# Optimization experiments

Hardware: AMD Instinct MI355X
Metric: run time of the kernel (lower is better)

The kernel has to match this reference:

```python
import jax, jax.numpy as jnp
import numpy as np

T, HID = 2048, 1536
H, DK, DV = 12, 128, 128
KEY_DIM, VAL_DIM = H * DK, H * DV
CONV_K, GEN_RED = 4, 8
EPS = 1e-5


def setup_inputs() -> dict:
    key = jax.random.key(0)
    ks = jax.random.split(key, 12)
    def rn(k, sh, scale):
        return jax.random.normal(k, sh, dtype=jnp.float32) * scale
    inv = HID ** -0.5
    return {
        "hidden_states": rn(ks[0], (T, HID), 1.0),
        "Wq": rn(ks[1], (HID, KEY_DIM), inv),
        "Wk": rn(ks[2], (HID, KEY_DIM), inv),
        "Wv": rn(ks[3], (HID, VAL_DIM), inv),
        "Wb": rn(ks[4], (HID, H), inv),
        "Wa": rn(ks[5], (HID, H), inv),
        "A_log": jnp.log(jax.random.uniform(ks[6], (H,), minval=1e-3, maxval=16.0)),
        "dt_bias": jnp.ones((H,), jnp.float32),
        "Wg1": rn(ks[7], (HID, HID // GEN_RED), inv),
        "Wg2": rn(ks[8], (HID // GEN_RED, VAL_DIM * CONV_K), (HID // GEN_RED) ** -0.5),
        "Wgate": rn(ks[9], (HID, VAL_DIM), inv),
        "norm_weight": jnp.ones((DV,), jnp.float32),
        "Wo": rn(ks[10], (VAL_DIM, HID), VAL_DIM ** -0.5),
    }


def _dynamic_conv(v, hs, Wg1, Wg2):
    # per-token per-channel causal depthwise conv; kernels generated from hidden_states
    w = jax.nn.silu(hs @ Wg1) @ Wg2                    # (T, VAL_DIM*K)
    w = w.reshape(T, VAL_DIM, CONV_K)                  # (T, D, K)
    vpad = jnp.pad(v, ((CONV_K - 1, 0), (0, 0)))       # causal left pad
    windows = jnp.stack([vpad[i:i + T] for i in range(CONV_K)], axis=1)  # (T, K, D)
    return jax.nn.silu(jnp.einsum('tkd,tdk->td', windows, w))


def _gated_delta_rule(q, k, v, g, beta):
    # q,k: (T,H,DK); v: (T,H,DV); g,beta: (T,H)
    scale = DK ** -0.5
    def step(S, inp):
        q_t, k_t, v_t, g_t, b_t = inp
        S = S * jnp.exp(g_t)[:, None, None]            # decay state
        kv = jnp.einsum('hk,hkv->hv', k_t, S)          # k^T S
        S = S + jnp.einsum('hk,hv->hkv', k_t, (v_t - kv) * b_t[:, None])
        o_t = jnp.einsum('hk,hkv->hv', q_t, S) * scale
        return S, o_t
    S0 = jnp.zeros((H, DK, DV), jnp.float32)
    _, o = jax.lax.scan(step, S0, (q, k, v, g, beta))
    return o                                           # (T, H, DV)


def reference(hidden_states, Wq, Wk, Wv, Wb, Wa, A_log, dt_bias,
              Wg1, Wg2, Wgate, norm_weight, Wo):
    hs = hidden_states
    q = jax.nn.silu(hs @ Wq).reshape(T, H, DK)
    k = jax.nn.silu(hs @ Wk).reshape(T, H, DK)
    v = _dynamic_conv(hs @ Wv, hs, Wg1, Wg2).reshape(T, H, DV)
    beta = jax.nn.sigmoid(hs @ Wb)                           # (T, H)
    g = -jnp.exp(A_log) * jax.nn.softplus(hs @ Wa + dt_bias)  # (T, H) log-decay
    o = _gated_delta_rule(q, k, v, g, beta)                  # (T, H, DV)
    # gated RMSNorm over head_v_dim
    gate = (hs @ Wgate).reshape(T, H, DV)
    o = o * jax.lax.rsqrt(jnp.mean(o * o, axis=-1, keepdims=True) + EPS)
    o = o * norm_weight * (gate * jax.nn.sigmoid(gate))
    return o.reshape(T, VAL_DIM) @ Wo
```

## Files before the change

kernel.cpp:

```cpp
#include <hip/hip_runtime.h>
#include <hip/hip_bf16.h>
#include <math.h>

#define T     2048
#define HID   1536
#define NH    12
#define DK    128
#define DV    128
#define CONVK 4
#define CH    64
#define NC    32

typedef __attribute__((ext_vector_type(8))) short bf16x8;
typedef __attribute__((ext_vector_type(8))) _Float16 fp16x8;
typedef __attribute__((ext_vector_type(4))) float floatx4;

__device__ __forceinline__ float siluf(float x) {
    return x / (1.0f + __expf(-x));
}
__device__ __forceinline__ unsigned short f2bf(float f) {
    union { __hip_bfloat16 b; unsigned short u; } cv;
    cv.b = __float2bfloat16(f);
    return cv.u;
}
__device__ __forceinline__ float bf2f(unsigned short u) {
    union { unsigned int u; float f; } cv;
    cv.u = ((unsigned int)u) << 16;
    return cv.f;
}
__device__ __forceinline__ unsigned short f2h(float f) {
    union { _Float16 h; unsigned short u; } cv;
    cv.h = (_Float16)f;
    return cv.u;
}
__device__ __forceinline__ void gl_lds16(const void* g, void* l) {
    __builtin_amdgcn_global_load_lds(
        (const __attribute__((address_space(1))) void*)g,
        (__attribute__((address_space(3))) void*)l, 16, 0, 0);
}
__device__ __forceinline__ void split8_store(const float* xv,
                                             unsigned short* dh, unsigned short* dl) {
    ushort4 h0, h1, l0, l1;
    h0.x = f2bf(xv[0]); l0.x = f2bf(xv[0] - bf2f(h0.x));
    h0.y = f2bf(xv[1]); l0.y = f2bf(xv[1] - bf2f(h0.y));
    h0.z = f2bf(xv[2]); l0.z = f2bf(xv[2] - bf2f(h0.z));
    h0.w = f2bf(xv[3]); l0.w = f2bf(xv[3] - bf2f(h0.w));
    h1.x = f2bf(xv[4]); l1.x = f2bf(xv[4] - bf2f(h1.x));
    h1.y = f2bf(xv[5]); l1.y = f2bf(xv[5] - bf2f(h1.y));
    h1.z = f2bf(xv[6]); l1.z = f2bf(xv[6] - bf2f(h1.z));
    h1.w = f2bf(xv[7]); l1.w = f2bf(xv[7] - bf2f(h1.w));
    *(ushort4*)dh = h0; *(ushort4*)(dh + 4) = h1;
    *(ushort4*)dl = l0; *(ushort4*)(dl + 4) = l1;
}

__global__ __launch_bounds__(256) void splitcast3_kernel(const float* __restrict__ s,
                                                         unsigned short* __restrict__ hi,
                                                         unsigned short* __restrict__ lo,
                                                         unsigned short* __restrict__ h16,
                                                         int n4) {
    int i = blockIdx.x * 256 + threadIdx.x;
    if (i >= n4) return;
    float4 x = ((const float4*)s)[i];
    ushort4 h, l, f;
    h.x = f2bf(x.x); l.x = f2bf(x.x - bf2f(h.x)); f.x = f2h(x.x);
    h.y = f2bf(x.y); l.y = f2bf(x.y - bf2f(h.y)); f.y = f2h(x.y);
    h.z = f2bf(x.z); l.z = f2bf(x.z - bf2f(h.z)); f.z = f2h(x.z);
    h.w = f2bf(x.w); l.w = f2bf(x.w - bf2f(h.w)); f.w = f2h(x.w);
    ((ushort4*)hi)[i] = h;
    ((ushort4*)lo)[i] = l;
    ((ushort4*)h16)[i] = f;
}

__global__ __launch_bounds__(256) void transsplit_kernel(const float* __restrict__ src,
                                                         unsigned short* __restrict__ hi,
                                                         unsigned short* __restrict__ lo,
                                                         int K, int N) {
    __shared__ float tile[32][33];
    const int k0 = blockIdx.y * 32, n0 = blockIdx.x * 32;
    const int tx = threadIdx.x, ty = threadIdx.y;
#pragma unroll
    for (int r = 0; r < 4; ++r) {
        int kk = k0 + ty + 8 * r, nn = n0 + tx;
        tile[ty + 8 * r][tx] = (nn < N) ? src[(size_t)kk * N + nn] : 0.0f;
    }
    __syncthreads();
#pragma unroll
    for (int r = 0; r < 4; ++r) {
        int nn = n0 + ty + 8 * r, kk = k0 + tx;
        if (nn < N) {
            float x = tile[tx][ty + 8 * r];
            unsigned short h = f2bf(x);
            hi[(size_t)nn * K + kk] = h;
            lo[(size_t)nn * K + kk] = f2bf(x - bf2f(h));
        }
    }
}

__global__ __launch_bounds__(256) void transcasth_kernel(const float* __restrict__ src,
                                                         unsigned short* __restrict__ dst,
                                                         int K, int N) {
    __shared__ float tile[32][33];
    const int k0 = blockIdx.y * 32, n0 = blockIdx.x * 32;
    const int tx = threadIdx.x, ty = threadIdx.y;
#pragma unroll
    for (int r = 0; r < 4; ++r) {
        int kk = k0 + ty + 8 * r, nn = n0 + tx;
        tile[ty + 8 * r][tx] = (nn < N) ? src[(size_t)kk * N + nn] : 0.0f;
    }
    __syncthreads();
#pragma unroll
    for (int r = 0; r < 4; ++r) {
        int nn = n0 + ty + 8 * r, kk = k0 + tx;
        if (nn < N) dst[(size_t)nn * K + kk] = f2h(tile[tx][ty + 8 * r]);
    }
}

template<int EPI, int MODE>
__global__ __launch_bounds__(256)
void mgemm(const unsigned short* __restrict__ Ah, const unsigned short* __restrict__ Al,
           const unsigned short* __restrict__ Bh, const unsigned short* __restrict__ Bl,
           int K, int N, float* __restrict__ C, unsigned short* __restrict__ Cb)
{
    constexpr int BN   = MODE ? 64 : 128;
    constexpr int BCH  = BN / 16;
    constexpr int NFR  = MODE ? 2 : 4;
    __shared__ unsigned short AsH[2][4096];
    __shared__ unsigned short BsH[2][BCH * 512];
    __shared__ unsigned short AsL[MODE ? 2 : 1][MODE ? 4096 : 4];
    __shared__ unsigned short BsL[MODE ? 2 : 1][MODE ? BCH * 512 : 4];
    const int tid = threadIdx.x;
    const int wave = tid >> 6, lane = tid & 63;
    const int wr = wave >> 1, wc = wave & 1;
    const int lm = lane & 15, lq = lane >> 4;
    const int rowBase = blockIdx.y * 128, colBase = blockIdx.x * BN;

    floatx4 acc[4][NFR];
#pragma unroll
    for (int i = 0; i < 4; ++i)
#pragma unroll
        for (int j = 0; j < NFR; ++j) acc[i][j] = (floatx4){0.f, 0.f, 0.f, 0.f};

    const int mt0 = wave * 2, mt1 = wave * 2 + 1;
    const size_t aOff0 = (size_t)(rowBase + mt0 * 16 + lm) * K + lq * 8;
    const size_t aOff1 = (size_t)(rowBase + mt1 * 16 + lm) * K + lq * 8;
    const size_t bOff0 = (size_t)(colBase + mt0 * 16 + lm) * K + lq * 8;
    const size_t bOff1 = (size_t)(colBase + mt1 * 16 + lm) * K + lq * 8;
    const size_t bOffW = (size_t)(colBase + wave * 16 + lm) * K + lq * 8;

    auto STAGE = [&](int buf, int k0) {
        gl_lds16(Ah + aOff0 + k0, &AsH[buf][mt0 * 512]);
        gl_lds16(Ah + aOff1 + k0, &AsH[buf][mt1 * 512]);
        if (MODE) {
            gl_lds16(Al + aOff0 + k0, &AsL[buf][mt0 * 512]);
            gl_lds16(Al + aOff1 + k0, &AsL[buf][mt1 * 512]);
            gl_lds16(Bh + bOffW + k0, &BsH[buf][wave * 512]);
            gl_lds16(Bl + bOffW + k0, &BsL[buf][wave * 512]);
        } else {
            gl_lds16(Bh + bOff0 + k0, &BsH[buf][mt0 * 512]);
            gl_lds16(Bh + bOff1 + k0, &BsH[buf][mt1 * 512]);
        }
    };

    const int nIter = K >> 5;
    STAGE(0, 0);
    __syncthreads();
    int cur = 0;
    for (int it = 0; it < nIter; ++it) {
        if (it + 1 < nIter) STAGE(cur ^ 1, (it + 1) << 5);
        if (MODE == 0) {
            fp16x8 a[4], b[4];
#pragma unroll
            for (int i = 0; i < 4; ++i) {
                a[i] = *(const fp16x8*)&AsH[cur][(wr * 4 + i) * 512 + lane * 8];
                b[i] = *(const fp16x8*)&BsH[cur][(wc * 4 + i) * 512 + lane * 8];
            }
#pragma unroll
            for (int mi = 0; mi < 4; ++mi)
#pragma unroll
                for (int ni = 0; ni < 4; ++ni)
                    acc[mi][ni] = __builtin_amdgcn_mfma_f32_16x16x32_f16(
                        a[mi], b[ni], acc[mi][ni], 0, 0, 0);
        } else {
            bf16x8 ah[4], al[4], bh[2], bl[2];
#pragma unroll
            for (int i = 0; i < 4; ++i) {
                ah[i] = *(const bf16x8*)&AsH[cur][(wr * 4 + i) * 512 + lane * 8];
                al[i] = *(const bf16x8*)&AsL[cur][(wr * 4 + i) * 512 + lane * 8];
            }
#pragma unroll
            for (int j = 0; j < 2; ++j) {
                bh[j] = *(const bf16x8*)&BsH[cur][(wc * 2 + j) * 512 + lane * 8];
                bl[j] = *(const bf16x8*)&BsL[cur][(wc * 2 + j) * 512 + lane * 8];
            }
#pragma unroll
            for (int mi = 0; mi < 4; ++mi)
#pragma unroll
                for (int ni = 0; ni < 2; ++ni) {
                    acc[mi][ni] = __builtin_amdgcn_mfma_f32_16x16x32_bf16(
                        ah[mi], bh[ni], acc[mi][ni], 0, 0, 0);
                    acc[mi][ni] = __builtin_amdgcn_mfma_f32_16x16x32_bf16(
                        al[mi], bh[ni], acc[mi][ni], 0, 0, 0);
                    acc[mi][ni] = __builtin_amdgcn_mfma_f32_16x16x32_bf16(
                        ah[mi], bl[ni], acc[mi][ni], 0, 0, 0);
                }
        }
        __syncthreads();
        cur ^= 1;
    }

#pragma unroll
    for (int mi = 0; mi < 4; ++mi)
#pragma unroll
        for (int ni = 0; ni < NFR; ++ni) {
            const int col = colBase + wc * (NFR * 16) + ni * 16 + lm;
#pragma unroll
            for (int r = 0; r < 4; ++r) {
                const int row = rowBase + wr * 64 + mi * 16 + lq * 4 + r;
                const float x = acc[mi][ni][r];
                if (EPI == 0) C[(size_t)row * N + col] = x;
                else          Cb[(size_t)row * N + col] = f2bf(x);
            }
        }
}

__global__ __launch_bounds__(256)
void mgemm_ab(const unsigned short* __restrict__ Ah0, const unsigned short* __restrict__ Bh0,
              const unsigned short* __restrict__ Ah1, const unsigned short* __restrict__ Al1,
              const unsigned short* __restrict__ Bh1, const unsigned short* __restrict__ Bl1,
              float* __restrict__ qf, float* __restrict__ vf,
              unsigned short* __restrict__ gsilb, unsigned short* __restrict__ w1h16,
              float* __restrict__ kf,
              const float* __restrict__ A_log, const float* __restrict__ dt_bias,
              float* __restrict__ beta, float* __restrict__ g)
{
    __shared__ unsigned short smem[24576];
    const int tid = threadIdx.x;
    const int wave = tid >> 6, lane = tid & 63;
    const int wr = wave >> 1, wc = wave & 1;
    const int lm = lane & 15, lq = lane >> 4;
    const int K = 1536;
    const int bx = blockIdx.x;

    bool roleA; int aidx = 0, bidx = 0;
    if (bx < 832) { roleA = ((bx & 1) == 0); aidx = bx >> 1; bidx = bx >> 1; }
    else          { roleA = true;            aidx = 416 + (bx - 832); }

    const int mt0 = wave * 2, mt1 = wave * 2 + 1;

    if (roleA) {
        const int rowBase = (aidx / 38) * 128, colBase = (aidx % 38) * 128;
        unsigned short* AsH = smem;
        unsigned short* BsH = smem + 8192;
        floatx4 acc[4][4];
#pragma unroll
        for (int i = 0; i < 4; ++i)
#pragma unroll
            for (int j = 0; j < 4; ++j) acc[i][j] = (floatx4){0.f, 0.f, 0.f, 0.f};

        const size_t aOff0 = (size_t)(rowBase + mt0 * 16 + lm) * K + lq * 8;
        const size_t aOff1 = (size_t)(rowBase + mt1 * 16 + lm) * K + lq * 8;
        const size_t bOff0 = (size_t)(colBase + mt0 * 16 + lm) * K + lq * 8;
        const size_t bOff1 = (size_t)(colBase + mt1 * 16 + lm) * K + lq * 8;

        auto STAGE = [&](int buf, int k0) {
            gl_lds16(Ah0 + aOff0 + k0, &AsH[buf * 4096 + mt0 * 512]);
            gl_lds16(Ah0 + aOff1 + k0, &AsH[buf * 4096 + mt1 * 512]);
            gl_lds16(Bh0 + bOff0 + k0, &BsH[buf * 4096 + mt0 * 512]);
// ... 222 lines not shown
    const int wave = tid >> 6, lane = tid & 63;
    const int lm = lane & 15, lq = lane >> 4;
    const int li = tid >> 2, lq4 = tid & 3;
    const size_t rowbase = (size_t)(c * CH) * HID + h * DK;

    {
        const float* ksrc = k + rowbase + (size_t)li * HID + lq4 * 32;
        const float* qsrc = q + rowbase + (size_t)li * HID + lq4 * 32;
        const float* vsrc = v + (size_t)(c * CH + li) * HID + h * DV + lq4 * 32;
#pragma unroll
        for (int f = 0; f < 8; ++f) {
            float4 kx = *(const float4*)(ksrc + f * 4);
            float4 qx = *(const float4*)(qsrc + f * 4);
            float4 vx = *(const float4*)(vsrc + f * 4);
            const int d0 = lq4 * 32 + f * 4;
            {
                ushort4 hh, ll;
                hh.x = f2bf(kx.x); ll.x = f2bf(kx.x - bf2f(hh.x));
                hh.y = f2bf(kx.y); ll.y = f2bf(kx.y - bf2f(hh.y));
                hh.z = f2bf(kx.z); ll.z = f2bf(kx.z - bf2f(hh.z));
                hh.w = f2bf(kx.w); ll.w = f2bf(kx.w - bf2f(hh.w));
                *(ushort4*)&KhS[li * 136 + d0] = hh;
                *(ushort4*)&KlS[li * 136 + d0] = ll;
            }
            {
                ushort4 hh, ll;
                hh.x = f2bf(qx.x); ll.x = f2bf(qx.x - bf2f(hh.x));
                hh.y = f2bf(qx.y); ll.y = f2bf(qx.y - bf2f(hh.y));
                hh.z = f2bf(qx.z); ll.z = f2bf(qx.z - bf2f(hh.z));
                hh.w = f2bf(qx.w); ll.w = f2bf(qx.w - bf2f(hh.w));
                *(ushort4*)&QhS[li * 136 + d0] = hh;
                *(ushort4*)&QlS[li * 136 + d0] = ll;
            }
            KT[(d0 + 0) * 68 + li] = kx.x;
            KT[(d0 + 1) * 68 + li] = kx.y;
            KT[(d0 + 2) * 68 + li] = kx.z;
            KT[(d0 + 3) * 68 + li] = kx.w;
            *(float4*)&Vs[li * 132 + d0] = vx;
        }
    }
    if (tid < 64) {
        float gv = g[(c * CH + tid) * NH + h];
        float bv = beta[(c * CH + tid) * NH + h];
        float csv = gv;
#pragma unroll
        for (int off = 1; off < 64; off <<= 1) {
            float n = __shfl_up(csv, off);
            if (tid >= off) csv += n;
        }
        cs[tid] = csv; sb[tid] = bv; sbb[tid] = bv * __expf(csv);
    }
    __syncthreads();

    {
        const int ti = wave;
#pragma unroll
        for (int tj = 0; tj < 4; ++tj) {
            floatx4 acc = (floatx4){0.f, 0.f, 0.f, 0.f};
#pragma unroll
            for (int ks = 0; ks < 4; ++ks) {
                bf16x8 a_h = *(const bf16x8*)&KhS[(ti * 16 + lm) * 136 + ks * 32 + lq * 8];
                bf16x8 a_l = *(const bf16x8*)&KlS[(ti * 16 + lm) * 136 + ks * 32 + lq * 8];
                bf16x8 b_h = *(const bf16x8*)&KhS[(tj * 16 + lm) * 136 + ks * 32 + lq * 8];
                bf16x8 b_l = *(const bf16x8*)&KlS[(tj * 16 + lm) * 136 + ks * 32 + lq * 8];
                acc = __builtin_amdgcn_mfma_f32_16x16x32_bf16(a_h, b_h, acc, 0, 0, 0);
                acc = __builtin_amdgcn_mfma_f32_16x16x32_bf16(a_h, b_l, acc, 0, 0, 0);
                acc = __builtin_amdgcn_mfma_f32_16x16x32_bf16(a_l, b_h, acc, 0, 0, 0);
            }
#pragma unroll
            for (int r = 0; r < 4; ++r) {
                const int i = ti * 16 + lq * 4 + r, j = tj * 16 + lm;
                As[i * 68 + j] = (j < i) ? sb[i] * __expf(cs[i] - cs[j]) * acc[r] : 0.0f;
            }
        }
        const size_t mbase = (size_t)(h * NC + c) * CH * CH;
#pragma unroll
        for (int tj = 0; tj < 4; ++tj) {
            floatx4 acc = (floatx4){0.f, 0.f, 0.f, 0.f};
#pragma unroll
            for (int ks = 0; ks < 4; ++ks) {
                bf16x8 a_h = *(const bf16x8*)&QhS[(ti * 16 + lm) * 136 + ks * 32 + lq * 8];
                bf16x8 a_l = *(const bf16x8*)&QlS[(ti * 16 + lm) * 136 + ks * 32 + lq * 8];
                bf16x8 b_h = *(const bf16x8*)&KhS[(tj * 16 + lm) * 136 + ks * 32 + lq * 8];
                bf16x8 b_l = *(const bf16x8*)&KlS[(tj * 16 + lm) * 136 + ks * 32 + lq * 8];
                acc = __builtin_amdgcn_mfma_f32_16x16x32_bf16(a_h, b_h, acc, 0, 0, 0);
                acc = __builtin_amdgcn_mfma_f32_16x16x32_bf16(a_h, b_l, acc, 0, 0, 0);
                acc = __builtin_amdgcn_mfma_f32_16x16x32_bf16(a_l, b_h, acc, 0, 0, 0);
            }
#pragma unroll
            for (int r = 0; r < 4; ++r) {
                const int i = ti * 16 + lq * 4 + r, j = tj * 16 + lm;
                Mg[mbase + (size_t)i * 64 + j] =
                    (j <= i) ? __expf(cs[i] - cs[j]) * acc[r] : 0.0f;
            }
        }
    }

    float xc[64];
    const int col = tid;
    if (col < 128) {
#pragma unroll
        for (int i = 0; i < 64; ++i) xc[i] = sb[i] * Vs[i * 132 + col];
    } else {
        const int dcol = col - 128;
#pragma unroll
        for (int i4 = 0; i4 < 16; ++i4) {
            float4 kq = *(const float4*)&KT[dcol * 68 + i4 * 4];
            xc[i4 * 4 + 0] = sbb[i4 * 4 + 0] * kq.x;
            xc[i4 * 4 + 1] = sbb[i4 * 4 + 1] * kq.y;
            xc[i4 * 4 + 2] = sbb[i4 * 4 + 2] * kq.z;
            xc[i4 * 4 + 3] = sbb[i4 * 4 + 3] * kq.w;
        }
    }
    __syncthreads();

#pragma unroll
    for (int i = 1; i < 64; ++i) {
        float a = xc[i];
#pragma unroll
        for (int j4 = 0; j4 < (i + 3) / 4; ++j4) {
            float4 a4 = *(const float4*)&As[i * 68 + j4 * 4];
            a -= a4.x * xc[j4 * 4 + 0] + a4.y * xc[j4 * 4 + 1]
               + a4.z * xc[j4 * 4 + 2] + a4.w * xc[j4 * 4 + 3];
        }
        xc[i] = a;
    }

    {
        const size_t xbase = (size_t)(h * NC + c) * CH * 128;
        if (col < 128) {
            for (int i = 0; i < 64; ++i) X1g[xbase + (size_t)i * 128 + col] = xc[i];
        } else {
            for (int i = 0; i < 64; ++i) Vs[i * 132 + (col - 128)] = xc[i];
        }
    }
    if (tid < 64) csg[(size_t)(h * NC + c) * CH + tid] = cs[tid];
    __syncthreads();

    const size_t tb = (size_t)(h * NC + c) * 8192;

    {
#pragma unroll
        for (int e = 0; e < 4; ++e) {
            int u = e * 256 + tid;
            int ch = u >> 6, l = u & 63;
            int i = (ch >> 2) * 16 + (l & 15);
            int dbase = (ch & 3) * 32 + (l >> 4) * 8;
            float4 a = *(const float4*)&Vs[i * 132 + dbase];
            float4 b = *(const float4*)&Vs[i * 132 + dbase + 4];
            float xv[8] = {-a.x, -a.y, -a.z, -a.w, -b.x, -b.y, -b.z, -b.w};
            split8_store(xv, &X2th[tb + ch * 512 + l * 8], &X2tl[tb + ch * 512 + l * 8]);
        }
    }

    {
#pragma unroll
        for (int e = 0; e < 4; ++e) {
            int u = e * 256 + tid;
            int ch = u >> 6, l = u & 63;
            int i = (ch >> 2) * 16 + (l & 15);
            int dbase = (ch & 3) * 32 + (l >> 4) * 8;
            *(bf16x8*)&Qth[tb + ch * 512 + l * 8] = *(const bf16x8*)&QhS[i * 136 + dbase];
            *(bf16x8*)&Qtl[tb + ch * 512 + l * 8] = *(const bf16x8*)&QlS[i * 136 + dbase];
        }
    }

    {
#pragma unroll
        for (int e = 0; e < 4; ++e) {
            int u = e * 256 + tid;
            int ch = u >> 6, l = u & 63;
            int dk = (ch >> 1) * 16 + (l & 15);
            int ibase = (ch & 1) * 32 + (l >> 4) * 8;
            float4 a = *(const float4*)&KT[dk * 68 + ibase];
            float4 b = *(const float4*)&KT[dk * 68 + ibase + 4];
            float xv[8] = {a.x, a.y, a.z, a.w, b.x, b.y, b.z, b.w};
            split8_store(xv, &Kth[tb + ch * 512 + l * 8], &Ktl[tb + ch * 512 + l * 8]);
        }
    }
}

struct StFrags {
    bf16x8 xh[4], xl[4], qh[4], ql[4], kh[4], kl[4];
    float x1r[4], csr[4], cs63;
};

__device__ __forceinline__ void st_load(
    StFrags& f,
    const unsigned short* __restrict__ Qth, const unsigned short* __restrict__ Qtl,
    const unsigned short* __restrict__ Kth, const unsigned short* __restrict__ Ktl,
    const unsigned short* __restrict__ X2th, const unsigned short* __restrict__ X2tl,
    const float* __restrict__ X1g, const float* __restrict__ csg,
    int h, int c, int db, int mw, int lane, int lq, int lm)
{
    const size_t hc = (size_t)(h * NC + c);
    const size_t xb = hc * CH * 128;
    const size_t tb = hc * 8192 + (size_t)lane * 8;
#pragma unroll
    for (int ks = 0; ks < 4; ++ks) {
        const size_t off = tb + (size_t)(mw * 4 + ks) * 512;
        f.xh[ks] = *(const bf16x8*)(X2th + off);
        f.xl[ks] = *(const bf16x8*)(X2tl + off);
        f.qh[ks] = *(const bf16x8*)(Qth + off);
        f.ql[ks] = *(const bf16x8*)(Qtl + off);
        f.kh[ks] = *(const bf16x8*)(Kth + off);
        f.kl[ks] = *(const bf16x8*)(Ktl + off);
    }
#pragma unroll
    for (int r = 0; r < 4; ++r) {
        const int row = mw * 16 + lq * 4 + r;
        f.x1r[r] = X1g[xb + (size_t)row * 128 + db * 16 + lm];
        f.csr[r] = csg[hc * CH + row];
    }
    f.cs63 = csg[hc * CH + 63];
}

__device__ __forceinline__ void st_compute(
    const StFrags& f, floatx4& st0, floatx4& st1,
    unsigned short* SBh, unsigned short* SBl,
    unsigned short* UBh, unsigned short* UBl,
    float* __restrict__ X1g, float* __restrict__ o,
    int h, int c, int db, int mw, int lane, int lq, int lm)
{
    const size_t hc = (size_t)(h * NC + c);
    const size_t xb = hc * CH * 128;

    {
        floatx4 aU0 = (floatx4){0.f, 0.f, 0.f, 0.f};
        floatx4 aU1 = (floatx4){0.f, 0.f, 0.f, 0.f};
        floatx4 aO0 = (floatx4){0.f, 0.f, 0.f, 0.f};
        floatx4 aO1 = (floatx4){0.f, 0.f, 0.f, 0.f};
#pragma unroll
        for (int ks = 0; ks < 4; ++ks) {
            bf16x8 sh = *(const bf16x8*)&SBh[lm * 136 + ks * 32 + lq * 8];
            bf16x8 sl = *(const bf16x8*)&SBl[lm * 136 + ks * 32 + lq * 8];
            if (ks & 1) {
                aU1 = __builtin_amdgcn_mfma_f32_16x16x32_bf16(f.xh[ks], sh, aU1, 0, 0, 0);
                aU1 = __builtin_amdgcn_mfma_f32_16x16x32_bf16(f.xh[ks], sl, aU1, 0, 0, 0);
                aU1 = __builtin_amdgcn_mfma_f32_16x16x32_bf16(f.xl[ks], sh, aU1, 0, 0, 0);
                aO1 = __builtin_amdgcn_mfma_f32_16x16x32_bf16(f.qh[ks], sh, aO1, 0, 0, 0);
                aO1 = __builtin_amdgcn_mfma_f32_16x16x32_bf16(f.qh[ks], sl, aO1, 0, 0, 0);
                aO1 = __builtin_amdgcn_mfma_f32_16x16x32_bf16(f.ql[ks], sh, aO1, 0, 0, 0);
            } else {
                aU0 = __builtin_amdgcn_mfma_f32_16x16x32_bf16(f.xh[ks], sh, aU0, 0, 0, 0);
                aU0 = __builtin_amdgcn_mfma_f32_16x16x32_bf16(f.xh[ks], sl, aU0, 0, 0, 0);
                aU0 = __builtin_amdgcn_mfma_f32_16x16x32_bf16(f.xl[ks], sh, aU0, 0, 0, 0);
                aO0 = __builtin_amdgcn_mfma_f32_16x16x32_bf16(f.qh[ks], sh, aO0, 0, 0, 0);
                aO0 = __builtin_amdgcn_mfma_f32_16x16x32_bf16(f.qh[ks], sl, aO0, 0, 0, 0);
                aO0 = __builtin_amdgcn_mfma_f32_16x16x32_bf16(f.ql[ks], sh, aO0, 0, 0, 0);
            }
        }
#pragma unroll
        for (int r = 0; r < 4; ++r) {
            const int row = mw * 16 + lq * 4 + r;
            const float u = aU0[r] + aU1[r] + f.x1r[r];
            X1g[xb + (size_t)row * 128 + db * 16 + lm] = u;
            const float up = u * __expf(f.cs63 - f.csr[r]);
            unsigned short uh = f2bf(up);
            UBh[lm * 72 + row] = uh;
            UBl[lm * 72 + row] = f2bf(up - bf2f(uh));
            o[(size_t)(c * CH + row) * HID + h * DV + db * 16 + lm] =
                __expf(f.csr[r]) * (aO0[r] + aO1[r]);
        }
    }
    __syncthreads();

    {
        const float bC = __expf(f.cs63);
#pragma unroll
        for (int mt2 = 0; mt2 < 2; ++mt2) {
            const int mt = mw * 2 + mt2;
            floatx4 acc;
            floatx4 stc = mt2 ? st1 : st0;
#pragma unroll
            for (int r = 0; r < 4; ++r) acc[r] = bC * stc[r];
#pragma unroll
            for (int ks = 0; ks < 2; ++ks) {
                bf16x8 ah = f.kh[mt2 * 2 + ks];
                bf16x8 al = f.kl[mt2 * 2 + ks];
                bf16x8 bh = *(const bf16x8*)&UBh[lm * 72 + ks * 32 + lq * 8];
                bf16x8 bl = *(const bf16x8*)&UBl[lm * 72 + ks * 32 + lq * 8];
                acc = __builtin_amdgcn_mfma_f32_16x16x32_bf16(ah, bh, acc, 0, 0, 0);
                acc = __builtin_amdgcn_mfma_f32_16x16x32_bf16(ah, bl, acc, 0, 0, 0);
                acc = __builtin_amdgcn_mfma_f32_16x16x32_bf16(al, bh, acc, 0, 0, 0);
            }
            if (mt2) st1 = acc; else st0 = acc;
            ushort4 shv, slv;
#pragma unroll
            for (int r = 0; r < 4; ++r) {
                const float sv = acc[r];
                unsigned short sh = f2bf(sv);
                ((unsigned short*)&shv)[r] = sh;
                ((unsigned short*)&slv)[r] = f2bf(sv - bf2f(sh));
            }
            const int dkb = mt * 16 + lq * 4;
            *(ushort4*)&SBh[lm * 136 + dkb] = shv;
            *(ushort4*)&SBl[lm * 136 + dkb] = slv;
        }
    }
    __syncthreads();
}

__global__ __launch_bounds__(256, 1) void state_kernel(
    const unsigned short* __restrict__ Qth, const unsigned short* __restrict__ Qtl,
    const unsigned short* __restrict__ Kth, const unsigned short* __restrict__ Ktl,
    const unsigned short* __restrict__ X2th, const unsigned short* __restrict__ X2tl,
    float* __restrict__ X1g ,
    const float* __restrict__ csg, float* __restrict__ o)
{
    __shared__ unsigned short SBh[16 * 136], SBl[16 * 136];
    __shared__ unsigned short UBh[16 * 72],  UBl[16 * 72];

    const int h = blockIdx.x, db = blockIdx.y;
    const int tid = threadIdx.x;
    const int mw = tid >> 6, lane = tid & 63;
    const int lm = lane & 15, lq = lane >> 4;

    for (int idx = tid; idx < 16 * 136; idx += 256) { SBh[idx] = 0; SBl[idx] = 0; }
    floatx4 st0 = (floatx4){0.f, 0.f, 0.f, 0.f};
    floatx4 st1 = (floatx4){0.f, 0.f, 0.f, 0.f};
    __syncthreads();

    StFrags fA, fB;
    st_load(fA, Qth, Qtl, Kth, Ktl, X2th, X2tl, X1g, csg, h, 0, db, mw, lane, lq, lm);
    for (int c = 0; c < NC; c += 2) {
        st_load(fB, Qth, Qtl, Kth, Ktl, X2th, X2tl, X1g, csg, h, c + 1, db, mw, lane, lq, lm);
        __builtin_amdgcn_sched_barrier(0);
        st_compute(fA, st0, st1, SBh, SBl, UBh, UBl, X1g, o, h, c, db, mw, lane, lq, lm);
        if (c + 2 < NC)
            st_load(fA, Qth, Qtl, Kth, Ktl, X2th, X2tl, X1g, csg, h, c + 2, db, mw, lane, lq, lm);
        __builtin_amdgcn_sched_barrier(0);
        st_compute(fB, st0, st1, SBh, SBl, UBh, UBl, X1g, o, h, c + 1, db, mw, lane, lq, lm);
    }
}

__global__ __launch_bounds__(256) void outk_kernel(
    const float* __restrict__ Ug, const float* __restrict__ Mg,
    float* __restrict__ o)
{
    __shared__ float Msh[64 * 68];
    __shared__ float Ush[64 * 68];

    const int c = blockIdx.x, h = blockIdx.y;
    const int dvb = blockIdx.z * 64;
    const int tid = threadIdx.x;
    const size_t hc = (size_t)(h * NC + c);

    for (int e = 0; e < 16; ++e) {
        int idx = e * 256 + tid;
        Msh[(idx >> 6) * 68 + (idx & 63)] = Mg[hc * CH * CH + idx];
    }
    for (int e = 0; e < 16; ++e) {
        int idx = e * 256 + tid;
        int j = idx >> 6, cc = idx & 63;
        Ush[j * 68 + cc] = Ug[hc * CH * 128 + (size_t)j * 128 + dvb + cc];
    }
    __syncthreads();

    const int tx = tid & 15, ty = tid >> 4;
    const int c0 = tx * 4, i0 = ty * 4;
    float acc[4][4] = {{0}};
    for (int j4 = 0; j4 < 16; ++j4) {
        float uv[4][4];
#pragma unroll
        for (int s = 0; s < 4; ++s) {
            float4 u4 = *(const float4*)&Ush[(j4 * 4 + s) * 68 + c0];
            uv[s][0] = u4.x; uv[s][1] = u4.y; uv[s][2] = u4.z; uv[s][3] = u4.w;
        }
#pragma unroll
        for (int r = 0; r < 4; ++r) {
            float4 m4 = *(const float4*)&Msh[(i0 + r) * 68 + j4 * 4];
            const float mv[4] = {m4.x, m4.y, m4.z, m4.w};
#pragma unroll
            for (int s = 0; s < 4; ++s)
#pragma unroll
                for (int e = 0; e < 4; ++e) acc[r][e] += mv[s] * uv[s][e];
        }
    }
    const float scale = 0.08838834764831845f;
#pragma unroll
    for (int r = 0; r < 4; ++r) {
        float* op = &o[(size_t)(c * CH + i0 + r) * HID + h * DV + dvb + c0];
        float4 prev = *(const float4*)op;
        float4 ov = make_float4(scale * (prev.x + acc[r][0]),
                                scale * (prev.y + acc[r][1]),
                                scale * (prev.z + acc[r][2]),
                                scale * (prev.w + acc[r][3]));
        *(float4*)op = ov;
    }
}

__global__ __launch_bounds__(256) void normgate_kernel(const float* __restrict__ o,
                                                       const unsigned short* __restrict__ gsil,
                                                       const float* __restrict__ nw,
                                                       unsigned short* __restrict__ out_hi,
                                                       unsigned short* __restrict__ out_lo) {
    const int gw = (blockIdx.x * 256 + threadIdx.x) >> 6;
    const int lane = threadIdx.x & 63;
    if (gw >= T * NH) return;
    const int t = gw / NH, h = gw % NH;
    const size_t base = (size_t)t * HID + h * DV;
    const float a = o[base + lane];
    const float b = o[base + lane + 64];
    float ss = a * a + b * b;
    ss += __shfl_xor(ss, 1);  ss += __shfl_xor(ss, 2);  ss += __shfl_xor(ss, 4);
    ss += __shfl_xor(ss, 8);  ss += __shfl_xor(ss, 16); ss += __shfl_xor(ss, 32);
    const float r = rsqrtf(ss * (1.0f / 128.0f) + 1e-5f);
    float va = a * r * nw[lane]      * bf2f(gsil[base + lane]);
    float vb = b * r * nw[lane + 64] * bf2f(gsil[base + lane + 64]);
    unsigned short ha = f2bf(va), hb = f2bf(vb);
    out_hi[base + lane]      = ha;  out_lo[base + lane]      = f2bf(va - bf2f(ha));
    out_hi[base + lane + 64] = hb;  out_lo[base + lane + 64] = f2bf(vb - bf2f(hb));
}

extern "C" void kernel_launch(void* const* d_in, const int* in_sizes, int n_in,
                              void* d_out, int out_size, void* d_ws, size_t ws_size,
                              hipStream_t stream) {
    const float* hs      = (const float*)d_in[0];
    const float* Wq      = (const float*)d_in[1];
    const float* Wk      = (const float*)d_in[2];
    const float* Wv      = (const float*)d_in[3];
    const float* Wb      = (const float*)d_in[4];
    const float* Wa      = (const float*)d_in[5];
    const float* A_log   = (const float*)d_in[6];
    const float* dt_bias = (const float*)d_in[7];
    const float* Wg1     = (const float*)d_in[8];
    const float* Wg2     = (const float*)d_in[9];
    const float* Wgate   = (const float*)d_in[10];
    const float* norm_w  = (const float*)d_in[11];
    const float* Wo      = (const float*)d_in[12];

    float* ws = (float*)d_ws;
    float* q    = ws;
    float* kbuf = ws + 3145728;
    float* vpre = ws + 6291456;
    float* vbuf = ws + 9437184;
    unsigned short* gsil = (unsigned short*)(ws + 12582912);
    float* X1g  = ws + 14155776;
    unsigned short* X2th = (unsigned short*)(ws + 17301504);
    unsigned short* X2tl = (unsigned short*)(ws + 18874368);
    float* Mg   = ws + 20447232;
    unsigned short* WTAfh = (unsigned short*)(ws + 14155776);
    unsigned short* WTBh  = (unsigned short*)(ws + 17891328);
    unsigned short* WTBl  = (unsigned short*)(ws + 19169280);
    unsigned short* WG2h  = (unsigned short*)(ws + 22044672);
    unsigned short* hsh   = (unsigned short*)(ws + 22634496);
    unsigned short* w1h16 = (unsigned short*)(ws + 24207360);
    unsigned short* Kth = (unsigned short*)(ws + 22044672);
    unsigned short* Ktl = (unsigned short*)(ws + 23617536);
    float* beta  = ws + 25190400;
    float* g     = ws + 25214976;
    float* csg   = ws + 25239552;
    unsigned short* hsbh = (unsigned short*)(ws + 9437184);
    unsigned short* hsbl = (unsigned short*)(ws + 11010048);
    unsigned short* Qth  = (unsigned short*)(ws + 6291456);
    unsigned short* Qtl  = (unsigned short*)(ws + 7864320);
    unsigned short* WoTh = (unsigned short*)(ws);
    unsigned short* WoTl = (unsigned short*)(ws + 1179648);
    unsigned short* onh  = (unsigned short*)(ws + 6291456);
    unsigned short* onl  = (unsigned short*)(ws + 7864320);

    const dim3 blk(256);
    const dim3 blkT(32, 8);

    splitcast3_kernel<<<3072, blk, 0, stream>>>(hs, hsbh, hsbl, hsh, (T * HID) / 4);
    transcasth_kernel<<<dim3(48, 48), blkT, 0, stream>>>(Wq,    WTAfh,               1536, 1536);
    transcasth_kernel<<<dim3(48, 48), blkT, 0, stream>>>(Wv,    WTAfh + 1536 * 1536, 1536, 1536);
    transcasth_kernel<<<dim3(48, 48), blkT, 0, stream>>>(Wgate, WTAfh + 3072 * 1536, 1536, 1536);
    transcasth_kernel<<<dim3(6, 48),  blkT, 0, stream>>>(Wg1,   WTAfh + 4608 * 1536, 1536, 192);
    transsplit_kernel<<<dim3(48, 48), blkT, 0, stream>>>(Wk, WTBh,               WTBl,               1536, 1536);
    transsplit_kernel<<<dim3(1, 48),  blkT, 0, stream>>>(Wb, WTBh + 1536 * 1536, WTBl + 1536 * 1536, 1536, 12);
    transsplit_kernel<<<dim3(1, 48),  blkT, 0, stream>>>(Wa, WTBh + 1548 * 1536, WTBl + 1548 * 1536, 1536, 12);
    transcasth_kernel<<<dim3(192, 6), blkT, 0, stream>>>(Wg2, WG2h, 192, 6144);

    mgemm_ab<<<1024, blk, 0, stream>>>(hsh, WTAfh, hsbh, hsbl, WTBh, WTBl,
                                       q, vpre, gsil, w1h16, kbuf,
                                       A_log, dt_bias, beta, g);

    convgemm<<<dim3(48, 16), blk, 0, stream>>>(w1h16, WG2h, vpre, vbuf);

    chunkloc_kernel<<<dim3(NC, NH), blk, 0, stream>>>(q, kbuf, vbuf, g, beta,
                                                      X1g, X2th, X2tl, Mg, csg,
                                                      Qth, Qtl, Kth, Ktl);
    state_kernel<<<dim3(NH, 8), blk, 0, stream>>>(Qth, Qtl, Kth, Ktl, X2th, X2tl,
                                                  X1g, csg, vbuf);
    transsplit_kernel<<<dim3(48, 48), blkT, 0, stream>>>(Wo, WoTh, WoTl, 1536, 1536);
    outk_kernel<<<dim3(NC, NH, 2), blk, 0, stream>>>(X1g, Mg, vbuf);

    normgate_kernel<<<6144, blk, 0, stream>>>(vbuf, gsil, norm_w, onh, onl);
    mgemm<0, 1><<<dim3(24, 16), blk, 0, stream>>>(onh, onl, WoTh, WoTl, 1536, 1536,
        (float*)d_out, nullptr);
}
```

Before: 551.6 us.

## Merge weight-prep launches into one kernel and fuse output correction with gated RMSNorm

The nine separate cast/transpose launches for hidden states and weights are folded into a single prep_all kernel that dispatches on block index ranges. The intra-chunk output correction kernel now covers the full 128-wide value dimension per block, so it can compute the RMS norm and gate in shared memory. That removes the separate normgate kernel and its round trip through global memory. In exchange, the output kernel launches half as many blocks, each using more registers and shared memory, which lowers parallelism.

Result: faster. 532.4 us (-3.5%).

```diff
diff --git a/kernel.cpp b/kernel.cpp
--- a/kernel.cpp
+++ b/kernel.cpp
@@ -53,66 +53,109 @@
     *(ushort4*)dl = l0; *(ushort4*)(dl + 4) = l1;
 }
 
-__global__ __launch_bounds__(256) void splitcast3_kernel(const float* __restrict__ s,
-                                                         unsigned short* __restrict__ hi,
-                                                         unsigned short* __restrict__ lo,
-                                                         unsigned short* __restrict__ h16,
-                                                         int n4) {
-    int i = blockIdx.x * 256 + threadIdx.x;
-    if (i >= n4) return;
-    float4 x = ((const float4*)s)[i];
-    ushort4 h, l, f;
-    h.x = f2bf(x.x); l.x = f2bf(x.x - bf2f(h.x)); f.x = f2h(x.x);
-    h.y = f2bf(x.y); l.y = f2bf(x.y - bf2f(h.y)); f.y = f2h(x.y);
-    h.z = f2bf(x.z); l.z = f2bf(x.z - bf2f(h.z)); f.z = f2h(x.z);
-    h.w = f2bf(x.w); l.w = f2bf(x.w - bf2f(h.w)); f.w = f2h(x.w);
-    ((ushort4*)hi)[i] = h;
-    ((ushort4*)lo)[i] = l;
-    ((ushort4*)h16)[i] = f;
+__device__ __forceinline__ void tch_body(const float* __restrict__ src,
+                                         unsigned short* __restrict__ dst,
+                                         int K, int N, int gx, int gy, int tid,
+                                         float* tile ) {
+    const int tx = tid & 31, ty = tid >> 5;
+    const int k0 = gy * 32, n0 = gx * 32;
+#pragma unroll
+    for (int r = 0; r < 4; ++r) {
+        int kk = k0 + ty + 8 * r, nn = n0 + tx;
+        tile[(ty + 8 * r) * 33 + tx] = (nn < N) ? src[(size_t)kk * N + nn] : 0.0f;
+    }
+    __syncthreads();
+#pragma unroll
+    for (int r = 0; r < 4; ++r) {
+        int nn = n0 + ty + 8 * r, kk = k0 + tx;
+        if (nn < N) dst[(size_t)nn * K + kk] = f2h(tile[tx * 33 + ty + 8 * r]);
+    }
+}
+__device__ __forceinline__ void tsp_body(const float* __restrict__ src,
+                                         unsigned short* __restrict__ hi,
+                                         unsigned short* __restrict__ lo,
+                                         int K, int N, int gx, int gy, int tid,
+                                         float* tile) {
+    const int tx = tid & 31, ty = tid >> 5;
+    const int k0 = gy * 32, n0 = gx * 32;
+#pragma unroll
+    for (int r = 0; r < 4; ++r) {
+        int kk = k0 + ty + 8 * r, nn = n0 + tx;
+        tile[(ty + 8 * r) * 33 + tx] = (nn < N) ? src[(size_t)kk * N + nn] : 0.0f;
+    }
+    __syncthreads();
+#pragma unroll
+    for (int r = 0; r < 4; ++r) {
+        int nn = n0 + ty + 8 * r, kk = k0 + tx;
+        if (nn < N) {
+            float x = tile[tx * 33 + ty + 8 * r];
+            unsigned short h = f2bf(x);
+            hi[(size_t)nn * K + kk] = h;
+            lo[(size_t)nn * K + kk] = f2bf(x - bf2f(h));
+        }
+    }
+}
+
+__global__ __launch_bounds__(256) void prep_all(
+    const float* __restrict__ hs,
+    unsigned short* __restrict__ hsbh, unsigned short* __restrict__ hsbl,
+    unsigned short* __restrict__ hsh,
+    const float* __restrict__ Wq, const float* __restrict__ Wv,
+    const float* __restrict__ Wgate, const float* __restrict__ Wg1,
+    const float* __restrict__ Wg2,
+    const float* __restrict__ Wk, const float* __restrict__ Wb,
+    const float* __restrict__ Wa,
+    unsigned short* __restrict__ WTAfh, unsigned short* __restrict__ WG2h,
+    unsigned short* __restrict__ WTBh, unsigned short* __restrict__ WTBl)
+{
+    __shared__ float tile[32 * 33];
+    const int bx = blockIdx.x, tid = threadIdx.x;
+
+    if (bx < 3072) {
+        const int i = bx * 256 + tid;
+        float4 x = ((const float4*)hs)[i];
+        ushort4 h, l, f;
+        h.x = f2bf(x.x); l.x = f2bf(x.x - bf2f(h.x)); f.x = f2h(x.x);
+        h.y = f2bf(x.y); l.y = f2bf(x.y - bf2f(h.y)); f.y = f2h(x.y);
+        h.z = f2bf(x.z); l.z = f2bf(x.z - bf2f(h.z)); f.z = f2h(x.z);
+        h.w = f2bf(x.w); l.w = f2bf(x.w - bf2f(h.w)); f.w = f2h(x.w);
+        ((ushort4*)hsbh)[i] = h;
+        ((ushort4*)hsbl)[i] = l;
+        ((ushort4*)hsh)[i]  = f;
+    } else if (bx < 5376) {
+        const int t = bx - 3072;
+        tch_body(Wq, WTAfh, 1536, 1536, t % 48, t / 48, tid, tile);
+    } else if (bx < 7680) {
+        const int t = bx - 5376;
+        tch_body(Wv, WTAfh + 1536 * 1536, 1536, 1536, t % 48, t / 48, tid, tile);
+    } else if (bx < 9984) {
+        const int t = bx - 7680;
+        tch_body(Wgate, WTAfh + 3072 * 1536, 1536, 1536, t % 48, t / 48, tid, tile);
+    } else if (bx < 10272) {
+        const int t = bx - 9984;
+        tch_body(Wg1, WTAfh + 4608 * 1536, 1536, 192, t % 6, t / 6, tid, tile);
+    } else if (bx < 11424) {
+        const int t = bx - 10272;
+        tch_body(Wg2, WG2h, 192, 6144, t % 192, t / 192, tid, tile);
+    } else if (bx < 13728) {
+        const int t = bx - 11424;
+        tsp_body(Wk, WTBh, WTBl, 1536, 1536, t % 48, t / 48, tid, tile);
+    } else if (bx < 13776) {
+        const int t = bx - 13728;
+        tsp_body(Wb, WTBh + 1536 * 1536, WTBl + 1536 * 1536, 1536, 12, 0, t, tid, tile);
+    } else {
+        const int t = bx - 13776;
+        tsp_body(Wa, WTBh + 1548 * 1536, WTBl + 1548 * 1536, 1536, 12, 0, t, tid, tile);
+    }
 }
 
 __global__ __launch_bounds__(256) void transsplit_kernel(const float* __restrict__ src,
                                                          unsigned short* __restrict__ hi,
                                                          unsigned short* __restrict__ lo,
                                                          int K, int N) {
-    __shared__ float tile[32][33];
-    const int k0 = blockIdx.y * 32, n0 = blockIdx.x * 32;
-    const int tx = threadIdx.x, ty = threadIdx.y;
-#pragma unroll
-    for (int r = 0; r < 4; ++r) {
-        int kk = k0 + ty + 8 * r, nn = n0 + tx;
-        tile[ty + 8 * r][tx] = (nn < N) ? src[(size_t)kk * N + nn] : 0.0f;
-    }
-    __syncthreads();
-#pragma unroll
-    for (int r = 0; r < 4; ++r) {
-        int nn = n0 + ty + 8 * r, kk = k0 + tx;
-        if (nn < N) {
-            float x = tile[tx][ty + 8 * r];
-            unsigned short h = f2bf(x);
-            hi[(size_t)nn * K + kk] = h;
-            lo[(size_t)nn * K + kk] = f2bf(x - bf2f(h));
-        }
-    }
-}
-
-__global__ __launch_bounds__(256) void transcasth_kernel(const float* __restrict__ src,
-                                                         unsigned short* __restrict__ dst,
-                                                         int K, int N) {
-    __shared__ float tile[32][33];
-    const int k0 = blockIdx.y * 32, n0 = blockIdx.x * 32;
-    const int tx = threadIdx.x, ty = threadIdx.y;
-#pragma unroll
-    for (int r = 0; r < 4; ++r) {
-        int kk = k0 + ty + 8 * r, nn = n0 + tx;
-        tile[ty + 8 * r][tx] = (nn < N) ? src[(size_t)kk * N + nn] : 0.0f;
-    }
-    __syncthreads();
-#pragma unroll
-    for (int r = 0; r < 4; ++r) {
-        int nn = n0 + ty + 8 * r, kk = k0 + tx;
-        if (nn < N) dst[(size_t)nn * K + kk] = f2h(tile[tx][ty + 8 * r]);
-    }
+    __shared__ float tile[32 * 33];
+    const int tid = (int)(threadIdx.y * blockDim.x + threadIdx.x);
+    tsp_body(src, hi, lo, K, N, blockIdx.x, blockIdx.y, tid, tile);
 }
 
 template<int EPI, int MODE>
@@ -641,7 +684,6 @@
             split8_store(xv, &X2th[tb + ch * 512 + l * 8], &X2tl[tb + ch * 512 + l * 8]);
         }
     }
-
     {
 #pragma unroll
         for (int e = 0; e < 4; ++e) {
@@ -653,7 +695,6 @@
             *(bf16x8*)&Qtl[tb + ch * 512 + l * 8] = *(const bf16x8*)&QlS[i * 136 + dbase];
         }
     }
-
     {
 #pragma unroll
         for (int e = 0; e < 4; ++e) {
@@ -794,8 +835,7 @@
     const unsigned short* __restrict__ Qth, const unsigned short* __restrict__ Qtl,
     const unsigned short* __restrict__ Kth, const unsigned short* __restrict__ Ktl,
     const unsigned short* __restrict__ X2th, const unsigned short* __restrict__ X2tl,
-    float* __restrict__ X1g ,
-    const float* __restrict__ csg, float* __restrict__ o)
+    float* __restrict__ X1g, const float* __restrict__ csg, float* __restrict__ o)
 {
     __shared__ unsigned short SBh[16 * 136], SBl[16 * 136];
     __shared__ unsigned short UBh[16 * 72],  UBl[16 * 72];
@@ -823,15 +863,17 @@
     }
 }
 
-__global__ __launch_bounds__(256) void outk_kernel(
+__global__ __launch_bounds__(256) void outknorm_kernel(
     const float* __restrict__ Ug, const float* __restrict__ Mg,
-    float* __restrict__ o)
+    const float* __restrict__ o ,
+    const unsigned short* __restrict__ gsil, const float* __restrict__ nw,
+    unsigned short* __restrict__ out_hi, unsigned short* __restrict__ out_lo)
 {
     __shared__ float Msh[64 * 68];
-    __shared__ float Ush[64 * 68];
+    __shared__ float Ush[64 * 132];
+    __shared__ float rsq[64];
 
     const int c = blockIdx.x, h = blockIdx.y;
-    const int dvb = blockIdx.z * 64;
     const int tid = threadIdx.x;
     const size_t hc = (size_t)(h * NC + c);
 
@@ -839,22 +881,24 @@
         int idx = e * 256 + tid;
         Msh[(idx >> 6) * 68 + (idx & 63)] = Mg[hc * CH * CH + idx];
     }
-    for (int e = 0; e < 16; ++e) {
+    for (int e = 0; e < 32; ++e) {
         int idx = e * 256 + tid;
-        int j = idx >> 6, cc = idx & 63;
-        Ush[j * 68 + cc] = Ug[hc * CH * 128 + (size_t)j * 128 + dvb + cc];
+        int j = idx >> 7, cc = idx & 127;
+        Ush[j * 132 + cc] = Ug[hc * CH * 128 + (size_t)j * 128 + cc];
     }
     __syncthreads();
 
     const int tx = tid & 15, ty = tid >> 4;
-    const int c0 = tx * 4, i0 = ty * 4;
-    float acc[4][4] = {{0}};
+    const int c0 = tx * 8, i0 = ty * 4;
+    float acc[4][8] = {{0}};
     for (int j4 = 0; j4 < 16; ++j4) {
-        float uv[4][4];
+        float uv[4][8];
 #pragma unroll
         for (int s = 0; s < 4; ++s) {
-            float4 u4 = *(const float4*)&Ush[(j4 * 4 + s) * 68 + c0];
-            uv[s][0] = u4.x; uv[s][1] = u4.y; uv[s][2] = u4.z; uv[s][3] = u4.w;
+            float4 u4a = *(const float4*)&Ush[(j4 * 4 + s) * 132 + c0];
+            float4 u4b = *(const float4*)&Ush[(j4 * 4 + s) * 132 + c0 + 4];
+            uv[s][0] = u4a.x; uv[s][1] = u4a.y; uv[s][2] = u4a.z; uv[s][3] = u4a.w;
+            uv[s][4] = u4b.x; uv[s][5] = u4b.y; uv[s][6] = u4b.z; uv[s][7] = u4b.w;
         }
 #pragma unroll
         for (int r = 0; r < 4; ++r) {
@@ -863,43 +907,47 @@
 #pragma unroll
             for (int s = 0; s < 4; ++s)
 #pragma unroll
-                for (int e = 0; e < 4; ++e) acc[r][e] += mv[s] * uv[s][e];
-        }
-    }
+                for (int e = 0; e < 8; ++e) acc[r][e] += mv[s] * uv[s][e];
+        }
+    }
+    __syncthreads();
+
     const float scale = 0.08838834764831845f;
 #pragma unroll
     for (int r = 0; r < 4; ++r) {
-        float* op = &o[(size_t)(c * CH + i0 + r) * HID + h * DV + dvb + c0];
-        float4 prev = *(const float4*)op;
-        float4 ov = make_float4(scale * (prev.x + acc[r][0]),
-                                scale * (prev.y + acc[r][1]),
-                                scale * (prev.z + acc[r][2]),
-                                scale * (prev.w + acc[r][3]));
-        *(float4*)op = ov;
-    }
-}
-
-__global__ __launch_bounds__(256) void normgate_kernel(const float* __restrict__ o,
-                                                       const unsigned short* __restrict__ gsil,
-                                                       const float* __restrict__ nw,
-                                                       unsigned short* __restrict__ out_hi,
-                                                       unsigned short* __restrict__ out_lo) {
-    const int gw = (blockIdx.x * 256 + threadIdx.x) >> 6;
-    const int lane = threadIdx.x & 63;
-    if (gw >= T * NH) return;
-    const int t = gw / NH, h = gw % NH;
-    const size_t base = (size_t)t * HID + h * DV;
-    const float a = o[base + lane];
-    const float b = o[base + lane + 64];
-    float ss = a * a + b * b;
-    ss += __shfl_xor(ss, 1);  ss += __shfl_xor(ss, 2);  ss += __shfl_xor(ss, 4);
-    ss += __shfl_xor(ss, 8);  ss += __shfl_xor(ss, 16); ss += __shfl_xor(ss, 32);
-    const float r = rsqrtf(ss * (1.0f / 128.0f) + 1e-5f);
-    float va = a * r * nw[lane]      * bf2f(gsil[base + lane]);
-    float vb = b * r * nw[lane + 64] * bf2f(gsil[base + lane + 64]);
-    unsigned short ha = f2bf(va), hb = f2bf(vb);
-    out_hi[base + lane]      = ha;  out_lo[base + lane]      = f2bf(va - bf2f(ha));
-    out_hi[base + lane + 64] = hb;  out_lo[base + lane + 64] = f2bf(vb - bf2f(hb));
+        const float* op = &o[(size_t)(c * CH + i0 + r) * HID + h * DV + c0];
+        float4 p0 = *(const float4*)op;
+        float4 p1 = *(const float4*)(op + 4);
+        const float pv[8] = {p0.x, p0.y, p0.z, p0.w, p1.x, p1.y, p1.z, p1.w};
+#pragma unroll
+        for (int e = 0; e < 8; ++e)
+            Ush[(i0 + r) * 132 + c0 + e] = scale * (pv[e] + acc[r][e]);
+    }
+    __syncthreads();
+
+    {
+        const int row = tid >> 2, sub = tid & 3;
+        float ss = 0.0f;
+#pragma unroll
+        for (int k2 = 0; k2 < 32; ++k2) {
+            float x = Ush[row * 132 + sub * 32 + k2];
+            ss += x * x;
+        }
+        ss += __shfl_xor(ss, 1);
+        ss += __shfl_xor(ss, 2);
+        if (sub == 0) rsq[row] = rsqrtf(ss * (1.0f / 128.0f) + 1e-5f);
+    }
+    __syncthreads();
+
+    for (int e = 0; e < 32; ++e) {
+        int idx = e * 256 + tid;
+        int j = idx >> 7, cc = idx & 127;
+        const size_t base = (size_t)(c * CH + j) * HID + h * DV;
+        float va = Ush[j * 132 + cc] * rsq[j] * nw[cc] * bf2f(gsil[base + cc]);
+        unsigned short ha = f2bf(va);
+        out_hi[base + cc] = ha;
+        out_lo[base + cc] = f2bf(va - bf2f(ha));
+    }
 }
 
 extern "C" void kernel_launch(void* const* d_in, const int* in_sizes, int n_in,
@@ -950,17 +998,10 @@
     unsigned short* onl  = (unsigned short*)(ws + 7864320);
 
     const dim3 blk(256);
-    const dim3 blkT(32, 8);
-
-    splitcast3_kernel<<<3072, blk, 0, stream>>>(hs, hsbh, hsbl, hsh, (T * HID) / 4);
-    transcasth_kernel<<<dim3(48, 48), blkT, 0, stream>>>(Wq,    WTAfh,               1536, 1536);
-    transcasth_kernel<<<dim3(48, 48), blkT, 0, stream>>>(Wv,    WTAfh + 1536 * 1536, 1536, 1536);
-    transcasth_kernel<<<dim3(48, 48), blkT, 0, stream>>>(Wgate, WTAfh + 3072 * 1536, 1536, 1536);
-    transcasth_kernel<<<dim3(6, 48),  blkT, 0, stream>>>(Wg1,   WTAfh + 4608 * 1536, 1536, 192);
-    transsplit_kernel<<<dim3(48, 48), blkT, 0, stream>>>(Wk, WTBh,               WTBl,               1536, 1536);
-    transsplit_kernel<<<dim3(1, 48),  blkT, 0, stream>>>(Wb, WTBh + 1536 * 1536, WTBl + 1536 * 1536, 1536, 12);
-    transsplit_kernel<<<dim3(1, 48),  blkT, 0, stream>>>(Wa, WTBh + 1548 * 1536, WTBl + 1548 * 1536, 1536, 12);
-    transcasth_kernel<<<dim3(192, 6), blkT, 0, stream>>>(Wg2, WG2h, 192, 6144);
+
+    prep_all<<<13824, blk, 0, stream>>>(hs, hsbh, hsbl, hsh,
+                                        Wq, Wv, Wgate, Wg1, Wg2, Wk, Wb, Wa,
+                                        WTAfh, WG2h, WTBh, WTBl);
 
     mgemm_ab<<<1024, blk, 0, stream>>>(hsh, WTAfh, hsbh, hsbl, WTBh, WTBl,
                                        q, vpre, gsil, w1h16, kbuf,
@@ -973,10 +1014,10 @@
                                                       Qth, Qtl, Kth, Ktl);
     state_kernel<<<dim3(NH, 8), blk, 0, stream>>>(Qth, Qtl, Kth, Ktl, X2th, X2tl,
                                                   X1g, csg, vbuf);
-    transsplit_kernel<<<dim3(48, 48), blkT, 0, stream>>>(Wo, WoTh, WoTl, 1536, 1536);
-    outk_kernel<<<dim3(NC, NH, 2), blk, 0, stream>>>(X1g, Mg, vbuf);
-
-    normgate_kernel<<<6144, blk, 0, stream>>>(vbuf, gsil, norm_w, onh, onl);
+    transsplit_kernel<<<dim3(48, 48), blk, 0, stream>>>(Wo, WoTh, WoTl, 1536, 1536);
+
+    outknorm_kernel<<<dim3(NC, NH), blk, 0, stream>>>(X1g, Mg, vbuf, gsil, norm_w,
+                                                      onh, onl);
     mgemm<0, 1><<<dim3(24, 16), blk, 0, stream>>>(onh, onl, WoTh, WoTl, 1536, 1536,
         (float*)d_out, nullptr);
 }
```
